# Kernel tuning notes

Hardware: AMD Instinct MI355X
Metric: run time of the kernel (lower is better)

The kernel has to match this reference:

```python
import jax, jax.numpy as jnp
import numpy as np

NUM_EXPERTS = 64
TOP_K = 2
TEMPERATURE = 1.0
MOMENTUM = 0.9


def _l2norm(x, axis=-1):
    # torch F.normalize: x / max(||x||, eps)
    n = jnp.linalg.norm(x, axis=axis, keepdims=True)
    return x / jnp.maximum(n, 1e-12)


def setup_inputs() -> dict:
    key = jax.random.key(0)
    k1, k2 = jax.random.split(key)
    hidden_states = jax.random.normal(k1, (4, 4096, 2048), dtype=jnp.float32)
    centers = _l2norm(jax.random.normal(k2, (NUM_EXPERTS, 2048), dtype=jnp.float32))
    return {"hidden_states": hidden_states, "centers": centers}


def reference(hidden_states, centers):
    B, T, H = hidden_states.shape
    flat = hidden_states.reshape(-1, H).astype(jnp.float32)  # [N, H]
    N = flat.shape[0]

    # cosine-similarity logits
    reps_n = _l2norm(flat)
    centers_n = _l2norm(centers)
    temp = jnp.maximum(jnp.float32(TEMPERATURE), 1e-6)
    logits = (reps_n @ centers_n.T) / temp  # [N, E]

    probs = jax.nn.softmax(logits, axis=-1)
    top_w, top_ids = jax.lax.top_k(probs, TOP_K)  # [N, k]
    top_w = top_w / (jnp.sum(top_w, axis=-1, keepdims=True) + 1e-9)

    # EMA center update from top-1 routed expert (training+update path)
    route = top_ids[:, 0]  # [N]
    sums = jax.ops.segment_sum(flat, route, num_segments=NUM_EXPERTS)  # [E, H]
    counts = jax.ops.segment_sum(jnp.ones((N, 1), jnp.float32), route,
                                 num_segments=NUM_EXPERTS)  # [E, 1]
    means = sums / (counts + 1e-6)
    updated = _l2norm(MOMENTUM * centers + (1.0 - MOMENTUM) * means)
    new_centers = jnp.where(counts > 0, updated, centers)

    top_ids = top_ids.reshape(B, T, TOP_K)
    top_w = top_w.reshape(B, T, TOP_K)
    return top_ids, top_w, new_centers
```

## Files before the change

kernel.cpp:

```cpp
#include <hip/hip_runtime.h>
#include <math.h>

#define NTOK 16384
#define HDIM 2048
#define NEXP 64
#define KK   32
#define TAU  5e-5f
#define MAXB 2048
#define TB   32
#define TPAD 36

typedef __attribute__((ext_vector_type(8))) short short8;
typedef __attribute__((ext_vector_type(4))) float f32x4;
typedef __attribute__((ext_vector_type(4))) unsigned int uint4v;


__global__ __launch_bounds__(256)
void zero_kernel(float* p, int n) {
  int i = blockIdx.x * 256 + threadIdx.x;
  if (i < n) p[i] = 0.0f;
}

__device__ __forceinline__ float block_reduce_sum(float v, float* red) {
  #pragma unroll
  for (int o = 32; o > 0; o >>= 1) v += __shfl_down(v, o, 64);
  int lane = threadIdx.x & 63;
  int wid  = threadIdx.x >> 6;
  if (lane == 0) red[wid] = v;
  __syncthreads();
  float s = red[0] + red[1] + red[2] + red[3];
  __syncthreads();
  return s;
}

__device__ __forceinline__ double block_reduce_sum_f64(double v, double* red) {
  const int tid = threadIdx.x;
  red[tid] = v;
  __syncthreads();
  if (tid < 128) red[tid] += red[tid + 128];
  __syncthreads();
  if (tid < 64)  red[tid] += red[tid + 64];
  __syncthreads();
  double s = 0.0;
  if (tid < 64) {
    s = red[tid];
    #pragma unroll
    for (int o = 32; o > 0; o >>= 1) s += __shfl_down(s, o, 64);
  }
  if (tid == 0) red[0] = s;
  __syncthreads();
  s = red[0];
  __syncthreads();
  return s;
}

__global__ __launch_bounds__(256)
void cnorm_kernel(const float* __restrict__ c, float* __restrict__ inv_nc) {
  __shared__ float red[4];
  int e = blockIdx.x;
  float ss = 0.f;
  #pragma unroll
  for (int j = 0; j < 8; ++j) {
    float v = c[e * HDIM + threadIdx.x + j * 256];
    ss += v * v;
  }
  float tot = block_reduce_sum(ss, red);
  if (threadIdx.x == 0) inv_nc[e] = 1.0f / fmaxf(sqrtf(tot), 1e-12f);
}

__global__ __launch_bounds__(256)
void cprep_kernel(const float* __restrict__ c, float* __restrict__ inv_nc,
                  float* __restrict__ bn, unsigned short* __restrict__ cbh,
                  unsigned short* __restrict__ cbl, int* __restrict__ zr) {
  __shared__ float red[4];
  __shared__ double redd[256];
  __shared__ float s_nc;
  const int e = blockIdx.x;
  const int tid = threadIdx.x;
  if (e == 0 && tid < 128) zr[tid] = 0;
  const float* cr = c + (size_t)e * HDIM;
  float ss = 0.f;
  double acc = 0.0;
  #pragma unroll
  for (int j = 0; j < 8; ++j) {
    float v = cr[tid + j * 256];
    ss += v * v;
    double dv = (double)v;
    acc += dv * dv;
  }
  float tot = block_reduce_sum(ss, red);
  double cn = block_reduce_sum_f64(acc, redd);
  if (tid == 0) {
    inv_nc[e] = 1.0f / fmaxf(sqrtf(tot), 1e-12f);
    s_nc = (float)fmax(sqrt(cn), 1e-12);
  }
  __syncthreads();
  const double nc = (double)s_nc;
  #pragma unroll
  for (int j = 0; j < 8; ++j) {
    const int k = tid + j * 256;
    const float v = cr[k];
    bn[(size_t)e * HDIM + k] = (float)((double)v / nc);
    unsigned u = __float_as_uint(v);
    unsigned h = u & 0xffff0000u;
    float r = v - __uint_as_float(h);
    cbh[(size_t)e * HDIM + k] = (unsigned short)(u >> 16);
    cbl[(size_t)e * HDIM + k] = (unsigned short)(__float_as_uint(r) >> 16);
  }
}

__device__ __forceinline__ void cvt2(float v0, float v1, unsigned &hi, unsigned &lo) {
  unsigned u0 = __float_as_uint(v0);
  unsigned u1 = __float_as_uint(v1);
  unsigned h0 = u0 & 0xffff0000u;
  unsigned h1 = u1 & 0xffff0000u;
  float r0 = v0 - __uint_as_float(h0);
  float r1 = v1 - __uint_as_float(h1);
  hi = (u0 >> 16) | h1;
  lo = (__float_as_uint(r0) >> 16) | (__float_as_uint(r1) & 0xffff0000u);
}

__global__ __launch_bounds__(256)
void fused_kernel(const float* __restrict__ x,
                  const unsigned short* __restrict__ cbh,
                  const unsigned short* __restrict__ cbl,
                  const float* __restrict__ inv_nc,
                  float* __restrict__ out, int* __restrict__ route,
                  int* __restrict__ nflag, int* __restrict__ flags) {
  __shared__ float lg[NEXP][TPAD];
  __shared__ float xn_lds[TB];
  __shared__ float snc[NEXP];

  const int tid  = threadIdx.x;
  const int t0   = blockIdx.x * TB;
  const int lane = tid & 63;
  const int w    = tid >> 6;
  const int tt   = (w & 1) * 16;
  const int eh   = (w >> 1) * 32;
  const int fr   = lane & 15;
  const int fk   = (lane >> 4) * 8;

  if (tid < NEXP) snc[tid] = inv_nc[tid];

  const float*          xa  = x   + (size_t)(t0 + tt + fr) * HDIM + fk;
  const unsigned short* b0h = cbh + (size_t)(eh + fr)      * HDIM + fk;
  const unsigned short* b0l = cbl + (size_t)(eh + fr)      * HDIM + fk;
  const unsigned short* b1h = cbh + (size_t)(eh + 16 + fr) * HDIM + fk;
  const unsigned short* b1l = cbl + (size_t)(eh + 16 + fr) * HDIM + fk;

  f32x4 acc0 = (f32x4){0.f, 0.f, 0.f, 0.f};
  f32x4 acc1 = (f32x4){0.f, 0.f, 0.f, 0.f};
  float nacc = 0.f;

  union U { uint4v u; short8 s; };

  f32x4  Aa0, Aa1, Ba0, Ba1, Ca0, Ca1, Da0, Da1;
  short8 Ah0, Al0, Ah1, Al1;
  short8 Bh0, Bl0, Bh1, Bl1;
  short8 Ch0, Cl0, Ch1, Cl1;
  short8 Dh0, Dl0, Dh1, Dl1;

  #define LDSLOT(S, i) do { const int o_ = (i) * KK;                      \
    S##a0 = *(const f32x4*)(xa + o_);                                     \
    S##a1 = *(const f32x4*)(xa + o_ + 4);                                 \
    S##h0 = *(const short8*)(b0h + o_);                                   \
    S##l0 = *(const short8*)(b0l + o_);                                   \
    S##h1 = *(const short8*)(b1h + o_);                                   \
    S##l1 = *(const short8*)(b1l + o_); } while (0)

  #define CONSUME(S) do {                                                 \
    unsigned h01_, l01_, h23_, l23_, h45_, l45_, h67_, l67_;              \
    cvt2(S##a0.x, S##a0.y, h01_, l01_);                                   \
    cvt2(S##a0.z, S##a0.w, h23_, l23_);                                   \
    cvt2(S##a1.x, S##a1.y, h45_, l45_);                                   \
    cvt2(S##a1.z, S##a1.w, h67_, l67_);                                   \
    U ah_; ah_.u = (uint4v){h01_, h23_, h45_, h67_};                      \
    U al_; al_.u = (uint4v){l01_, l23_, l45_, l67_};                      \
    nacc += S##a0.x*S##a0.x + S##a0.y*S##a0.y + S##a0.z*S##a0.z + S##a0.w*S##a0.w \
          + S##a1.x*S##a1.x + S##a1.y*S##a1.y + S##a1.z*S##a1.z + S##a1.w*S##a1.w; \
    acc0 = __builtin_amdgcn_mfma_f32_16x16x32_bf16(ah_.s, S##h0, acc0, 0, 0, 0); \
    acc0 = __builtin_amdgcn_mfma_f32_16x16x32_bf16(ah_.s, S##l0, acc0, 0, 0, 0); \
    acc0 = __builtin_amdgcn_mfma_f32_16x16x32_bf16(al_.s, S##h0, acc0, 0, 0, 0); \
    acc1 = __builtin_amdgcn_mfma_f32_16x16x32_bf16(ah_.s, S##h1, acc1, 0, 0, 0); \
    acc1 = __builtin_amdgcn_mfma_f32_16x16x32_bf16(ah_.s, S##l1, acc1, 0, 0, 0); \
    acc1 = __builtin_amdgcn_mfma_f32_16x16x32_bf16(al_.s, S##h1, acc1, 0, 0, 0); \
  } while (0)

  LDSLOT(A, 0);
  LDSLOT(B, 1);
  LDSLOT(C, 2);

  #pragma unroll 1
  for (int it = 0; it < 64; it += 4) {
    LDSLOT(D, it + 3);
    CONSUME(A);
    if (it + 4 < 64) LDSLOT(A, it + 4);
    CONSUME(B);
    if (it + 5 < 64) LDSLOT(B, it + 5);
    CONSUME(C);
    if (it + 6 < 64) LDSLOT(C, it + 6);
    CONSUME(D);
  }
  #undef LDSLOT
  #undef CONSUME

  float s = nacc;
  s += __shfl_xor(s, 16, 64);
  s += __shfl_xor(s, 32, 64);
  if (lane < 16) xn_lds[tt + lane] = s;

  const int tb = tt + (lane >> 4) * 4;
  *(f32x4*)&lg[eh + fr][tb]      = acc0;
  *(f32x4*)&lg[eh + 16 + fr][tb] = acc1;
  __syncthreads();

  if (tid < TB) {
    const int t  = tid;
    const int tg = t0 + t;
    const float inv_nx = 1.0f / fmaxf(sqrtf(xn_lds[t]), 1e-12f);
    float m1 = -1e30f, m2 = -1e30f, m3 = -1e30f;
    int i1 = 0, i2 = 0;
    #pragma unroll
    for (int e = 0; e < NEXP; ++e) {
      float l = lg[e][t] * snc[e] * inv_nx;
      if (l > m1)      { m3 = m2; m2 = m1; i2 = i1; m1 = l; i1 = e; }
      else if (l > m2) { m3 = m2; m2 = l; i2 = e; }
      else if (l > m3) { m3 = l; }
    }
    float Z = 0.f;
    #pragma unroll
    for (int e = 0; e < NEXP; ++e)
      Z += expf(lg[e][t] * snc[e] * inv_nx - m1);
    const float p1w = 1.0f / Z;
    const float p2w = expf(m2 - m1) / Z;
    const float s2  = p1w + p2w + 1e-9f;
    out[tg * 2 + 0] = (float)i1;
    out[tg * 2 + 1] = (float)i2;
    out[2 * NTOK + tg * 2 + 0] = p1w / s2;
    out[2 * NTOK + tg * 2 + 1] = p2w / s2;
    route[tg] = i1;
    if ((m1 - m2) < TAU || (m2 - m3) < TAU) {
      int idx = atomicAdd(nflag, 1);
      flags[idx] = tg;
    }
  }
}

__global__ __launch_bounds__(256)
void refine_np_kernel(const float* __restrict__ x, const float* __restrict__ bn,
                      float* __restrict__ out, int* __restrict__ route,
                      const int* __restrict__ nflag, const int* __restrict__ flags) {
  __shared__ float a_lds[HDIM];
  __shared__ double redd[256];
  __shared__ float lf[NEXP];
  __shared__ float s_nx;
  const int tid  = threadIdx.x;
  const int lane = tid & 63;
  const int w    = tid >> 6;
  const int n = *nflag;
  for (int j = blockIdx.x; j < n; j += gridDim.x) {
    const int t = flags[j];
    const float* xr = x + (size_t)t * HDIM;
    double xacc = 0.0;
    #pragma unroll
    for (int i = 0; i < 8; ++i) {
      double v = (double)xr[tid + 256 * i];
      xacc += v * v;
    }
    double xn = block_reduce_sum_f64(xacc, redd);
    if (tid == 0) s_nx = (float)fmax(sqrt(xn), 1e-12);
    __syncthreads();
    const double nx = (double)s_nx;
    #pragma unroll
    for (int i = 0; i < 8; ++i) {
      int k = tid + 256 * i;
      a_lds[k] = (float)((double)xr[k] / nx);
    }
    __syncthreads();
    #pragma unroll 1
    for (int ei = 0; ei < 16; ++ei) {
      const int e = w * 16 + ei;
      const float* br = bn + (size_t)e * HDIM;
      double d = 0.0;
      #pragma unroll 8
      for (int i = 0; i < 32; ++i) {
        int k = lane + 64 * i;
        d += (double)a_lds[k] * (double)br[k];
      }
      #pragma unroll
      for (int o = 32; o > 0; o >>= 1) d += __shfl_down(d, o, 64);
      if (lane == 0) lf[e] = (float)d;
    }
    __syncthreads();
    if (tid == 0) {
      float m32 = lf[0];
      for (int ee = 1; ee < NEXP; ++ee) m32 = fmaxf(m32, lf[ee]);
      float ex[NEXP];
      for (int ee = 0; ee < NEXP; ++ee)
        ex[ee] = (float)exp((double)(lf[ee] - m32));
      float r[8];
      #pragma unroll
      for (int q = 0; q < 8; ++q) r[q] = ex[q];
      for (int i = 8; i < NEXP; i += 8)
        #pragma unroll
        for (int q = 0; q < 8; ++q) r[q] += ex[i + q];
      const float Z = ((r[0] + r[1]) + (r[2] + r[3])) + ((r[4] + r[5]) + (r[6] + r[7]));
      float p1 = -1.f, p2 = -1.f;
      int i1 = 0, i2 = 0;
      for (int ee = 0; ee < NEXP; ++ee) {
        float p = ex[ee] / Z;
        if (p > p1)      { p2 = p1; i2 = i1; p1 = p; i1 = ee; }
        else if (p > p2) { p2 = p; i2 = ee; }
      }
      const float s = (p1 + p2) + 1e-9f;
      out[t * 2 + 0] = (float)i1;
      out[t * 2 + 1] = (float)i2;
      out[2 * NTOK + t * 2 + 0] = p1 / s;
      out[2 * NTOK + t * 2 + 1] = p2 / s;
      route[t] = i1;
    }
    __syncthreads();
  }
}

__global__ __launch_bounds__(64)
void refine_np_slow(const float* __restrict__ x, const float* __restrict__ c,
                    float* __restrict__ out, int* __restrict__ route,
                    const int* __restrict__ nflag, const int* __restrict__ flags) {
  __shared__ float lf[NEXP];
  const int e = threadIdx.x;
  const int n = *nflag;
  for (int j = blockIdx.x; j < n; j += gridDim.x) {
    const int t = flags[j];
    const float* xr = x + (size_t)t * HDIM;
    const float* cr = c + (size_t)e * HDIM;
    double xn = 0.0, cn = 0.0;
    for (int k = 0; k < HDIM; ++k) {
      double xv = (double)xr[k];
      double cv = (double)cr[k];
      xn += xv * xv;
      cn += cv * cv;
    }
    const float nx32 = (float)fmax(sqrt(xn), 1e-12);
    const float nc32 = (float)fmax(sqrt(cn), 1e-12);
    double d = 0.0;
    for (int k = 0; k < HDIM; ++k) {
      float a = (float)((double)xr[k] / (double)nx32);
      float b = (float)((double)cr[k] / (double)nc32);
      d += (double)a * (double)b;
    }
    lf[e] = (float)d;
    __syncthreads();
    if (e == 0) {
      float m32 = lf[0];
      for (int ee = 1; ee < NEXP; ++ee) m32 = fmaxf(m32, lf[ee]);
      float ex[NEXP];
      for (int ee = 0; ee < NEXP; ++ee)
        ex[ee] = (float)exp((double)(lf[ee] - m32));
      float r[8];
      #pragma unroll
      for (int q = 0; q < 8; ++q) r[q] = ex[q];
      for (int i = 8; i < NEXP; i += 8)
        #pragma unroll
        for (int q = 0; q < 8; ++q) r[q] += ex[i + q];
      const float Z = ((r[0] + r[1]) + (r[2] + r[3])) + ((r[4] + r[5]) + (r[6] + r[7]));
      float p1 = -1.f, p2 = -1.f;
      int i1 = 0, i2 = 0;
      for (int ee = 0; ee < NEXP; ++ee) {
        float p = ex[ee] / Z;
        if (p > p1)      { p2 = p1; i2 = i1; p1 = p; i1 = ee; }
        else if (p > p2) { p2 = p; i2 = ee; }
      }
      const float s = (p1 + p2) + 1e-9f;
      out[t * 2 + 0] = (float)i1;
      out[t * 2 + 1] = (float)i2;
      out[2 * NTOK + t * 2 + 0] = p1 / s;
      out[2 * NTOK + t * 2 + 1] = p2 / s;
      route[t] = i1;
    }
    __syncthreads();
  }
}

__global__ __launch_bounds__(256)
void scatter_kernel(const int* __restrict__ route, int* __restrict__ cursor,
                    int* __restrict__ bucket) {
  const int t = blockIdx.x * 256 + threadIdx.x;
  const int e = route[t];
  const int pos = atomicAdd(&cursor[e], 1);
  if (pos < MAXB) bucket[e * MAXB + pos] = t;
}

__global__ __launch_bounds__(256)
void segsum_part(const float* __restrict__ x, const int* __restrict__ cursor,
                 const int* __restrict__ bucket, float* __restrict__ psum) {
  __shared__ f32x4 part[4][64];
  const int e   = blockIdx.x >> 5;
  const int hc  = (blockIdx.x >> 2) & 7;
  const int ts  = blockIdx.x & 3;
  const int hb  = hc * 256;
  const int tid = threadIdx.x;
  const int rg  = tid >> 6;
  const int cc  = tid & 63;
  int n = cursor[e];
  if (n > MAXB) n = MAXB;
  const int nq = (n + 3) >> 2;
  const int lo = ts * nq;
  const int hi = min(lo + nq, n);
  const int* bk = bucket + e * MAXB;
  f32x4 a = (f32x4){0.f, 0.f, 0.f, 0.f};
  #pragma unroll 4
  for (int i = lo + rg; i < hi; i += 4)
    a += *(const f32x4*)(x + (size_t)bk[i] * HDIM + hb + cc * 4);
  part[rg][cc] = a;
  __syncthreads();
  if (tid < 64) {
    f32x4 s = part[0][tid] + part[1][tid] + part[2][tid] + part[3][tid];
    *(f32x4*)&psum[(size_t)(ts * NEXP + e) * HDIM + hb + tid * 4] = s;
  }
}

__global__ __launch_bounds__(256)
void finalize4_kernel(const float* __restrict__ c, const float* __restrict__ psum,
                      const int* __restrict__ counts, float* __restrict__ out) {
  __shared__ float red[4];
  const int e = blockIdx.x;
  const int tid = threadIdx.x;
  const float cnt = (float)counts[e];
  const float minv = 1.0f / (cnt + 1e-6f);
  float u[8], cv[8];
  float ss = 0.f;
  #pragma unroll
  for (int j = 0; j < 8; ++j) {
    int h = tid + j * 256;
    cv[j] = c[e * HDIM + h];
    float sm = psum[(size_t)(0 * NEXP + e) * HDIM + h]
             + psum[(size_t)(1 * NEXP + e) * HDIM + h]
             + psum[(size_t)(2 * NEXP + e) * HDIM + h]
             + psum[(size_t)(3 * NEXP + e) * HDIM + h];
    float mean = sm * minv;
    u[j] = 0.9f * cv[j] + 0.1f * mean;
    ss += u[j] * u[j];
  }
  float tot = block_reduce_sum(ss, red);
  float sc = 1.0f / fmaxf(sqrtf(tot), 1e-12f);
  const bool nz = cnt > 0.f;
  #pragma unroll
  for (int j = 0; j < 8; ++j) {
    int h = tid + j * 256;
    out[4 * NTOK + e * HDIM + h] = nz ? u[j] * sc : cv[j];
  }
}

__global__ __launch_bounds__(256)
void finalize_kernel(const float* __restrict__ c, const float* __restrict__ sums,
                     const int* __restrict__ counts, float* __restrict__ out) {
  __shared__ float red[4];
  const int e = blockIdx.x;
  const int tid = threadIdx.x;
  const float cnt = (float)counts[e];
  const float minv = 1.0f / (cnt + 1e-6f);
  float u[8], cv[8];
  float ss = 0.f;
  #pragma unroll
  for (int j = 0; j < 8; ++j) {
    int h = tid + j * 256;
    cv[j] = c[e * HDIM + h];
    float mean = sums[e * HDIM + h] * minv;
    u[j] = 0.9f * cv[j] + 0.1f * mean;
    ss += u[j] * u[j];
  }
  float tot = block_reduce_sum(ss, red);
  float sc = 1.0f / fmaxf(sqrtf(tot), 1e-12f);
  const bool nz = cnt > 0.f;
  #pragma unroll
  for (int j = 0; j < 8; ++j) {
    int h = tid + j * 256;
    out[4 * NTOK + e * HDIM + h] = nz ? u[j] * sc : cv[j];
  }
}

__global__ __launch_bounds__(256)
void router_kernel(const float* __restrict__ x, const float* __restrict__ c,
                   const float* __restrict__ inv_nc, float* __restrict__ out,
                   int* __restrict__ route, int* __restrict__ nflag,
                   int* __restrict__ flags) {
  __shared__ __align__(16) float xs[64][36];
  __shared__ float lgs[64][67];
  const int tid  = threadIdx.x;
  const int lane = tid & 63;
  const int w    = tid >> 6;
  const int t0   = blockIdx.x * 64;
  const int e0   = __builtin_amdgcn_readfirstlane(w * 16);
  const float* cb = c + (size_t)e0 * HDIM;
  const int st = tid >> 3;
  const int sk = (tid & 7) * 4;
  float acc[16];
  #pragma unroll
  for (int e = 0; e < 16; ++e) acc[e] = 0.f;
  float nacc = 0.f;
  float4 p0 = *(const float4*)&x[(size_t)(t0 + st)      * HDIM + sk];
  float4 p1 = *(const float4*)&x[(size_t)(t0 + st + 32) * HDIM + sk];
  for (int k0 = 0; k0 < HDIM; k0 += 32) {
    __syncthreads();
    *(float4*)&xs[st][sk]      = p0;
    *(float4*)&xs[st + 32][sk] = p1;
    __syncthreads();
    const int kn = k0 + 32;
    if (kn < HDIM) {
      p0 = *(const float4*)&x[(size_t)(t0 + st)      * HDIM + kn + sk];
      p1 = *(const float4*)&x[(size_t)(t0 + st + 32) * HDIM + kn + sk];
    }
    float a[32];
    #pragma unroll
    for (int j = 0; j < 32; j += 4) {
      float4 v = *(const float4*)&xs[lane][j];
      a[j] = v.x; a[j+1] = v.y; a[j+2] = v.z; a[j+3] = v.w;
    }
    if (w == 0) {
      #pragma unroll
      for (int j = 0; j < 32; ++j) nacc += a[j] * a[j];
    }
    #pragma unroll
    for (int e = 0; e < 16; ++e) {
      const float* br = cb + (size_t)e * HDIM + k0;
      #pragma unroll
      for (int j = 0; j < 32; j += 4) {
        float4 bv = *(const float4*)&br[j];
        acc[e] += a[j]*bv.x + a[j+1]*bv.y + a[j+2]*bv.z + a[j+3]*bv.w;
      }
    }
  }
  #pragma unroll
  for (int e = 0; e < 16; ++e) lgs[lane][e0 + e] = acc[e] * inv_nc[e0 + e];
  __syncthreads();
  if (w == 0) {
    const float inv_nx = 1.0f / fmaxf(sqrtf(nacc), 1e-12f);
    float m1 = -1e30f, m2 = -1e30f, m3 = -1e30f;
    int i1 = 0, i2 = 0;
    for (int e = 0; e < NEXP; ++e) {
      float l = lgs[lane][e] * inv_nx;
      if (l > m1)      { m3 = m2; m2 = m1; i2 = i1; m1 = l; i1 = e; }
      else if (l > m2) { m3 = m2; m2 = l; i2 = e; }
      else if (l > m3) { m3 = l; }
    }
    float Z = 0.f;
    for (int e = 0; e < NEXP; ++e) Z += expf(lgs[lane][e] * inv_nx - m1);
    const float p1w = 1.0f / Z;
    const float p2w = expf(m2 - m1) / Z;
    const float s   = p1w + p2w + 1e-9f;
    const int tg = t0 + lane;
    out[tg * 2 + 0] = (float)i1;
    out[tg * 2 + 1] = (float)i2;
    out[2 * NTOK + tg * 2 + 0] = p1w / s;
    out[2 * NTOK + tg * 2 + 1] = p2w / s;
    route[tg] = i1;
    if ((m1 - m2) < TAU || (m2 - m3) < TAU) {
      int idx = atomicAdd(nflag, 1);
      flags[idx] = tg;
    }
  }
}

__global__ __launch_bounds__(512)
void segsum_kernel(const float* __restrict__ x, const int* __restrict__ route,
                   float* __restrict__ sums, int* __restrict__ counts) {
  __shared__ float ls[NEXP * 256];
  __shared__ int lcnt[NEXP];
  const int tid  = threadIdx.x;
  const int lane = tid & 63;
  const int w    = tid >> 6;
  const int hc   = blockIdx.x & 7;
  const int tg   = blockIdx.x >> 3;
  const int hb   = hc * 256;
  #pragma unroll
  for (int i = 0; i < 32; ++i) ls[tid + i * 512] = 0.f;
  if (tid < NEXP) lcnt[tid] = 0;
  __syncthreads();
  const int tbase = tg * 512 + w * 64;
  #pragma unroll 4
  for (int i = 0; i < 64; ++i) {
    const int t = tbase + i;
    const int e = route[t];
    const float* xr = x + (size_t)t * HDIM + hb + lane;
    #pragma unroll
    for (int j = 0; j < 4; ++j)
      atomicAdd(&ls[e * 256 + lane + 64 * j], xr[64 * j]);
    if (hc == 0 && lane == 0) atomicAdd(&lcnt[e], 1);
  }
  __syncthreads();
  #pragma unroll
  for (int i = tid; i < NEXP * 256; i += 512) {
    const int e = i >> 8, h = i & 255;
    atomicAdd(&sums[e * HDIM + hb + h], ls[i]);
  }
  if (hc == 0 && tid < NEXP && lcnt[tid] > 0) atomicAdd(&counts[tid], lcnt[tid]);
}

extern "C" void kernel_launch(void* const* d_in, const int* in_sizes, int n_in,
                              void* d_out, int out_size, void* d_ws, size_t ws_size,
                              hipStream_t stream) {
  const float* x = (const float*)d_in[0];
  const float* c = (const float*)d_in[1];
  float* out = (float*)d_out;
  float* ws = (float*)d_ws;

  float* inv_nc = ws;
  int*   counts = (int*)(ws + 64);
  int*   nflag  = (int*)(ws + 128);
  int*   route  = (int*)(ws + 192);
  int*   flags  = (int*)(ws + 16576);
  float* sums   = ws + 32960;
  float* bn     = ws + 164032;
  unsigned short* cbh = (unsigned short*)(ws + 295104);
  unsigned short* cbl = (unsigned short*)(ws + 360640);
  int*   bucket = (int*)(ws + 426176);
  float* psum   = ws + 557248;

  const size_t NEED = 1081536ull * 4ull;
  if (ws_size >= NEED) {
    cprep_kernel<<<NEXP, 256, 0, stream>>>(c, inv_nc, bn, cbh, cbl, counts);
    fused_kernel<<<NTOK / TB, 256, 0, stream>>>(x, cbh, cbl, inv_nc, out, route, nflag, flags);
    refine_np_kernel<<<512, 256, 0, stream>>>(x, bn, out, route, nflag, flags);
    scatter_kernel<<<64, 256, 0, stream>>>(route, counts, bucket);
    segsum_part<<<2048, 256, 0, stream>>>(x, counts, bucket, psum);
    finalize4_kernel<<<NEXP, 256, 0, stream>>>(c, psum, counts, out);
  } else {
    zero_kernel<<<1, 256, 0, stream>>>(ws + 64, 128);
    zero_kernel<<<512, 256, 0, stream>>>(sums, 131072);
    cnorm_kernel<<<NEXP, 256, 0, stream>>>(c, inv_nc);
    router_kernel<<<NTOK / 64, 256, 0, stream>>>(x, c, inv_nc, out, route, nflag, flags);
    refine_np_slow<<<1024, 64, 0, stream>>>(x, c, out, route, nflag, flags);
    segsum_kernel<<<256, 512, 0, stream>>>(x, route, sums, counts);
    finalize_kernel<<<NEXP, 256, 0, stream>>>(c, sums, counts, out);
  }
}
```

Measured before the change: 346.3 us.

## Stage GEMM operands through double-buffered LDS and fuse bucket scatter into router

The fused router kernel now loads x and the split-bf16 centers into double-buffered shared memory, with 16 tokens per 128-thread block, so each center tile is shared across waves instead of being fetched per wave straight from global memory. It adds a __syncthreads on every K step. The separate scatter kernel is removed: the router appends each token to its expert bucket with atomics, and the refine kernel moves a token between buckets by tombstoning its old slot (-1) and fixing separate counts. This saves a launch and a pass over route, but adds per-iteration barriers, contended atomics in the router, and a branch in segsum.

Result: faster. 310.3 us (-10.4%).

```diff
diff --git a/kernel.cpp b/kernel.cpp
--- a/kernel.cpp
+++ b/kernel.cpp
@@ -7,12 +7,13 @@
 #define KK   32
 #define TAU  5e-5f
 #define MAXB 2048
-#define TB   32
-#define TPAD 36
+#define TB   16
+#define KPAD 40
+#define TPAD 20
 
 typedef __attribute__((ext_vector_type(8))) short short8;
 typedef __attribute__((ext_vector_type(4))) float f32x4;
-typedef __attribute__((ext_vector_type(4))) unsigned int uint4v;
+typedef __attribute__((ext_vector_type(2))) unsigned int uint2v;
 
 
 __global__ __launch_bounds__(256)
@@ -71,13 +72,15 @@
 __global__ __launch_bounds__(256)
 void cprep_kernel(const float* __restrict__ c, float* __restrict__ inv_nc,
                   float* __restrict__ bn, unsigned short* __restrict__ cbh,
-                  unsigned short* __restrict__ cbl, int* __restrict__ zr) {
+                  unsigned short* __restrict__ cbl, int* __restrict__ zr,
+                  int* __restrict__ cnt) {
   __shared__ float red[4];
   __shared__ double redd[256];
   __shared__ float s_nc;
   const int e = blockIdx.x;
   const int tid = threadIdx.x;
   if (e == 0 && tid < 128) zr[tid] = 0;
+  if (e == 1 && tid < 64)  cnt[tid] = 0;
   const float* cr = c + (size_t)e * HDIM;
   float ss = 0.f;
   double acc = 0.0;
@@ -120,96 +123,102 @@
   lo = (__float_as_uint(r0) >> 16) | (__float_as_uint(r1) & 0xffff0000u);
 }
 
-__global__ __launch_bounds__(256)
+__global__ __launch_bounds__(128)
 void fused_kernel(const float* __restrict__ x,
                   const unsigned short* __restrict__ cbh,
                   const unsigned short* __restrict__ cbl,
                   const float* __restrict__ inv_nc,
                   float* __restrict__ out, int* __restrict__ route,
-                  int* __restrict__ nflag, int* __restrict__ flags) {
+                  int* __restrict__ nflag, int* __restrict__ flags,
+                  int* __restrict__ cursor, int* __restrict__ cnt,
+                  int* __restrict__ bucket, int* __restrict__ posa) {
+  __shared__ __align__(16) unsigned short Ah[2][TB][KPAD];
+  __shared__ __align__(16) unsigned short Al[2][TB][KPAD];
+  __shared__ __align__(16) unsigned short Bh[2][NEXP][KPAD];
+  __shared__ __align__(16) unsigned short Bl[2][NEXP][KPAD];
   __shared__ float lg[NEXP][TPAD];
   __shared__ float xn_lds[TB];
   __shared__ float snc[NEXP];
 
   const int tid  = threadIdx.x;
   const int t0   = blockIdx.x * TB;
+  const int sr   = tid >> 3;
+  const int sq   = (tid & 7) * 4;
+  const int er   = tid >> 1;
+  const int eq   = (tid & 1) * 16;
   const int lane = tid & 63;
   const int w    = tid >> 6;
-  const int tt   = (w & 1) * 16;
-  const int eh   = (w >> 1) * 32;
+  const int eh   = w * 32;
   const int fr   = lane & 15;
   const int fk   = (lane >> 4) * 8;
 
   if (tid < NEXP) snc[tid] = inv_nc[tid];
 
-  const float*          xa  = x   + (size_t)(t0 + tt + fr) * HDIM + fk;
-  const unsigned short* b0h = cbh + (size_t)(eh + fr)      * HDIM + fk;
-  const unsigned short* b0l = cbl + (size_t)(eh + fr)      * HDIM + fk;
-  const unsigned short* b1h = cbh + (size_t)(eh + 16 + fr) * HDIM + fk;
-  const unsigned short* b1l = cbl + (size_t)(eh + 16 + fr) * HDIM + fk;
+  const float*          xptr = x   + (size_t)(t0 + sr) * HDIM + sq;
+  const unsigned short* bh_p = cbh + (size_t)er * HDIM + eq;
+  const unsigned short* bl_p = cbl + (size_t)er * HDIM + eq;
+
+  f32x4 xp;
+  short8 bh0r, bh1r, bl0r, bl1r;
+  float nacc = 0.f;
+
+  auto stage = [&](int b) {
+    unsigned h01, l01, h23, l23;
+    cvt2(xp.x, xp.y, h01, l01);
+    cvt2(xp.z, xp.w, h23, l23);
+    *(uint2v*)&Ah[b][sr][sq] = (uint2v){h01, h23};
+    *(uint2v*)&Al[b][sr][sq] = (uint2v){l01, l23};
+    nacc += xp.x*xp.x + xp.y*xp.y + xp.z*xp.z + xp.w*xp.w;
+    *(short8*)&Bh[b][er][eq]     = bh0r;
+    *(short8*)&Bh[b][er][eq + 8] = bh1r;
+    *(short8*)&Bl[b][er][eq]     = bl0r;
+    *(short8*)&Bl[b][er][eq + 8] = bl1r;
+  };
+  auto ldreg = [&](int it) {
+    const int o = it * KK;
+    xp   = *(const f32x4*)(xptr + o);
+    bh0r = *(const short8*)(bh_p + o);
+    bh1r = *(const short8*)(bh_p + o + 8);
+    bl0r = *(const short8*)(bl_p + o);
+    bl1r = *(const short8*)(bl_p + o + 8);
+  };
+
+  ldreg(0);
+  stage(0);
+  ldreg(1);
+  __syncthreads();
 
   f32x4 acc0 = (f32x4){0.f, 0.f, 0.f, 0.f};
   f32x4 acc1 = (f32x4){0.f, 0.f, 0.f, 0.f};
-  float nacc = 0.f;
-
-  union U { uint4v u; short8 s; };
-
-  f32x4  Aa0, Aa1, Ba0, Ba1, Ca0, Ca1, Da0, Da1;
-  short8 Ah0, Al0, Ah1, Al1;
-  short8 Bh0, Bl0, Bh1, Bl1;
-  short8 Ch0, Cl0, Ch1, Cl1;
-  short8 Dh0, Dl0, Dh1, Dl1;
-
-  #define LDSLOT(S, i) do { const int o_ = (i) * KK;                      \
-    S##a0 = *(const f32x4*)(xa + o_);                                     \
-    S##a1 = *(const f32x4*)(xa + o_ + 4);                                 \
-    S##h0 = *(const short8*)(b0h + o_);                                   \
-    S##l0 = *(const short8*)(b0l + o_);                                   \
-    S##h1 = *(const short8*)(b1h + o_);                                   \
-    S##l1 = *(const short8*)(b1l + o_); } while (0)
-
-  #define CONSUME(S) do {                                                 \
-    unsigned h01_, l01_, h23_, l23_, h45_, l45_, h67_, l67_;              \
-    cvt2(S##a0.x, S##a0.y, h01_, l01_);                                   \
-    cvt2(S##a0.z, S##a0.w, h23_, l23_);                                   \
-    cvt2(S##a1.x, S##a1.y, h45_, l45_);                                   \
-    cvt2(S##a1.z, S##a1.w, h67_, l67_);                                   \
-    U ah_; ah_.u = (uint4v){h01_, h23_, h45_, h67_};                      \
-    U al_; al_.u = (uint4v){l01_, l23_, l45_, l67_};                      \
-    nacc += S##a0.x*S##a0.x + S##a0.y*S##a0.y + S##a0.z*S##a0.z + S##a0.w*S##a0.w \
-          + S##a1.x*S##a1.x + S##a1.y*S##a1.y + S##a1.z*S##a1.z + S##a1.w*S##a1.w; \
-    acc0 = __builtin_amdgcn_mfma_f32_16x16x32_bf16(ah_.s, S##h0, acc0, 0, 0, 0); \
-    acc0 = __builtin_amdgcn_mfma_f32_16x16x32_bf16(ah_.s, S##l0, acc0, 0, 0, 0); \
-    acc0 = __builtin_amdgcn_mfma_f32_16x16x32_bf16(al_.s, S##h0, acc0, 0, 0, 0); \
-    acc1 = __builtin_amdgcn_mfma_f32_16x16x32_bf16(ah_.s, S##h1, acc1, 0, 0, 0); \
-    acc1 = __builtin_amdgcn_mfma_f32_16x16x32_bf16(ah_.s, S##l1, acc1, 0, 0, 0); \
-    acc1 = __builtin_amdgcn_mfma_f32_16x16x32_bf16(al_.s, S##h1, acc1, 0, 0, 0); \
-  } while (0)
-
-  LDSLOT(A, 0);
-  LDSLOT(B, 1);
-  LDSLOT(C, 2);
-
-  #pragma unroll 1
-  for (int it = 0; it < 64; it += 4) {
-    LDSLOT(D, it + 3);
-    CONSUME(A);
-    if (it + 4 < 64) LDSLOT(A, it + 4);
-    CONSUME(B);
-    if (it + 5 < 64) LDSLOT(B, it + 5);
-    CONSUME(C);
-    if (it + 6 < 64) LDSLOT(C, it + 6);
-    CONSUME(D);
-  }
-  #undef LDSLOT
-  #undef CONSUME
+
+  for (int it = 0; it < 64; ++it) {
+    const int cur = it & 1;
+    short8 ah  = *(const short8*)&Ah[cur][fr][fk];
+    short8 al  = *(const short8*)&Al[cur][fr][fk];
+    short8 bh0 = *(const short8*)&Bh[cur][eh + fr][fk];
+    short8 bl0 = *(const short8*)&Bl[cur][eh + fr][fk];
+    short8 bh1 = *(const short8*)&Bh[cur][eh + 16 + fr][fk];
+    short8 bl1 = *(const short8*)&Bl[cur][eh + 16 + fr][fk];
+    if (it < 63) {
+      stage(cur ^ 1);
+      if (it < 62) ldreg(it + 2);
+    }
+    acc0 = __builtin_amdgcn_mfma_f32_16x16x32_bf16(ah, bh0, acc0, 0, 0, 0);
+    acc0 = __builtin_amdgcn_mfma_f32_16x16x32_bf16(ah, bl0, acc0, 0, 0, 0);
+    acc0 = __builtin_amdgcn_mfma_f32_16x16x32_bf16(al, bh0, acc0, 0, 0, 0);
+    acc1 = __builtin_amdgcn_mfma_f32_16x16x32_bf16(ah, bh1, acc1, 0, 0, 0);
+    acc1 = __builtin_amdgcn_mfma_f32_16x16x32_bf16(ah, bl1, acc1, 0, 0, 0);
+    acc1 = __builtin_amdgcn_mfma_f32_16x16x32_bf16(al, bh1, acc1, 0, 0, 0);
+    __syncthreads();
+  }
 
   float s = nacc;
-  s += __shfl_xor(s, 16, 64);
-  s += __shfl_xor(s, 32, 64);
-  if (lane < 16) xn_lds[tt + lane] = s;
-
-  const int tb = tt + (lane >> 4) * 4;
+  s += __shfl_xor(s, 1, 64);
+  s += __shfl_xor(s, 2, 64);
+  s += __shfl_xor(s, 4, 64);
+  if ((tid & 7) == 0) xn_lds[sr] = s;
+
+  const int tb = (lane >> 4) * 4;
   *(f32x4*)&lg[eh + fr][tb]      = acc0;
   *(f32x4*)&lg[eh + 16 + fr][tb] = acc1;
   __syncthreads();
@@ -239,6 +248,10 @@
     out[2 * NTOK + tg * 2 + 0] = p1w / s2;
     out[2 * NTOK + tg * 2 + 1] = p2w / s2;
     route[tg] = i1;
+    const int p = atomicAdd(&cursor[i1], 1);
+    atomicAdd(&cnt[i1], 1);
+    if (p < MAXB) bucket[i1 * MAXB + p] = tg;
+    posa[tg] = p;
     if ((m1 - m2) < TAU || (m2 - m3) < TAU) {
       int idx = atomicAdd(nflag, 1);
       flags[idx] = tg;
@@ -249,7 +262,9 @@
 __global__ __launch_bounds__(256)
 void refine_np_kernel(const float* __restrict__ x, const float* __restrict__ bn,
                       float* __restrict__ out, int* __restrict__ route,
-                      const int* __restrict__ nflag, const int* __restrict__ flags) {
+                      const int* __restrict__ nflag, const int* __restrict__ flags,
+                      int* __restrict__ cursor, int* __restrict__ cnt,
+                      int* __restrict__ bucket, int* __restrict__ posa) {
   __shared__ float a_lds[HDIM];
   __shared__ double redd[256];
   __shared__ float lf[NEXP];
@@ -317,7 +332,17 @@
       out[t * 2 + 1] = (float)i2;
       out[2 * NTOK + t * 2 + 0] = p1 / s;
       out[2 * NTOK + t * 2 + 1] = p2 / s;
-      route[t] = i1;
+      const int old = route[t];
+      if (i1 != old) {
+        const int p_old = posa[t];
+        if (p_old < MAXB) bucket[old * MAXB + p_old] = -1;
+        atomicSub(&cnt[old], 1);
+        const int p = atomicAdd(&cursor[i1], 1);
+        atomicAdd(&cnt[i1], 1);
+        if (p < MAXB) bucket[i1 * MAXB + p] = t;
+        posa[t] = p;
+        route[t] = i1;
+      }
     }
     __syncthreads();
   }
@@ -383,15 +408,6 @@
 }
 
 __global__ __launch_bounds__(256)
-void scatter_kernel(const int* __restrict__ route, int* __restrict__ cursor,
-                    int* __restrict__ bucket) {
-  const int t = blockIdx.x * 256 + threadIdx.x;
-  const int e = route[t];
-  const int pos = atomicAdd(&cursor[e], 1);
-  if (pos < MAXB) bucket[e * MAXB + pos] = t;
-}
-
-__global__ __launch_bounds__(256)
 void segsum_part(const float* __restrict__ x, const int* __restrict__ cursor,
                  const int* __restrict__ bucket, float* __restrict__ psum) {
   __shared__ f32x4 part[4][64];
@@ -410,8 +426,10 @@
   const int* bk = bucket + e * MAXB;
   f32x4 a = (f32x4){0.f, 0.f, 0.f, 0.f};
   #pragma unroll 4
-  for (int i = lo + rg; i < hi; i += 4)
-    a += *(const f32x4*)(x + (size_t)bk[i] * HDIM + hb + cc * 4);
+  for (int i = lo + rg; i < hi; i += 4) {
+    const int r = bk[i];
+    if (r >= 0) a += *(const f32x4*)(x + (size_t)r * HDIM + hb + cc * 4);
+  }
   part[rg][cc] = a;
   __syncthreads();
   if (tid < 64) {
@@ -606,7 +624,7 @@
   float* ws = (float*)d_ws;
 
   float* inv_nc = ws;
-  int*   counts = (int*)(ws + 64);
+  int*   cursor = (int*)(ws + 64);
   int*   nflag  = (int*)(ws + 128);
   int*   route  = (int*)(ws + 192);
   int*   flags  = (int*)(ws + 16576);
@@ -616,22 +634,25 @@
   unsigned short* cbl = (unsigned short*)(ws + 360640);
   int*   bucket = (int*)(ws + 426176);
   float* psum   = ws + 557248;
-
-  const size_t NEED = 1081536ull * 4ull;
+  int*   posa   = (int*)(ws + 1081536);
+  int*   cnt    = (int*)(ws + 1097920);
+
+  const size_t NEED = 1097984ull * 4ull;
   if (ws_size >= NEED) {
-    cprep_kernel<<<NEXP, 256, 0, stream>>>(c, inv_nc, bn, cbh, cbl, counts);
-    fused_kernel<<<NTOK / TB, 256, 0, stream>>>(x, cbh, cbl, inv_nc, out, route, nflag, flags);
-    refine_np_kernel<<<512, 256, 0, stream>>>(x, bn, out, route, nflag, flags);
-    scatter_kernel<<<64, 256, 0, stream>>>(route, counts, bucket);
-    segsum_part<<<2048, 256, 0, stream>>>(x, counts, bucket, psum);
-    finalize4_kernel<<<NEXP, 256, 0, stream>>>(c, psum, counts, out);
+    cprep_kernel<<<NEXP, 256, 0, stream>>>(c, inv_nc, bn, cbh, cbl, cursor, cnt);
+    fused_kernel<<<NTOK / TB, 128, 0, stream>>>(x, cbh, cbl, inv_nc, out, route,
+                                                nflag, flags, cursor, cnt, bucket, posa);
+    refine_np_kernel<<<512, 256, 0, stream>>>(x, bn, out, route, nflag, flags,
+                                              cursor, cnt, bucket, posa);
+    segsum_part<<<2048, 256, 0, stream>>>(x, cursor, bucket, psum);
+    finalize4_kernel<<<NEXP, 256, 0, stream>>>(c, psum, cnt, out);
   } else {
     zero_kernel<<<1, 256, 0, stream>>>(ws + 64, 128);
     zero_kernel<<<512, 256, 0, stream>>>(sums, 131072);
     cnorm_kernel<<<NEXP, 256, 0, stream>>>(c, inv_nc);
     router_kernel<<<NTOK / 64, 256, 0, stream>>>(x, c, inv_nc, out, route, nflag, flags);
     refine_np_slow<<<1024, 64, 0, stream>>>(x, c, out, route, nflag, flags);
-    segsum_kernel<<<256, 512, 0, stream>>>(x, route, sums, counts);
-    finalize_kernel<<<NEXP, 256, 0, stream>>>(c, sums, counts, out);
-  }
-}
+    segsum_kernel<<<256, 512, 0, stream>>>(x, route, sums, cursor);
+    finalize_kernel<<<NEXP, 256, 0, stream>>>(c, sums, cursor, out);
+  }
+}
```
